# Performance work log

Hardware: AMD Instinct MI355X
Metric: run time of the kernel (lower is better)

## Reference

```python
import jax, jax.numpy as jnp
import numpy as np

B, H, NQ, NK, D = 256, 16, 49, 49, 64
SCALE = 1.0 / np.sqrt(D).astype(np.float32)
EPS = 1e-9  # matches kernel's 1/(l + 1e-9)


def setup_inputs() -> dict:
    key = jax.random.key(0)
    kq, kk, kv = jax.random.split(key, 3)
    q = jax.random.normal(kq, (B, H, NQ, D), dtype=jnp.float32)
    k = jax.random.normal(kk, (B, H, NK, D), dtype=jnp.float32)
    v = jax.random.normal(kv, (B, H, NK, D), dtype=jnp.float32)
    return {"q": q, "k": k, "v": v}


def reference(q, k, v):
    # scores: [B,H,Nq,Nk]
    s = jnp.einsum("bhqd,bhkd->bhqk", q, k) * SCALE
    m = jnp.max(s, axis=-1, keepdims=True)
    e = jnp.exp(s - m)
    l = jnp.sum(e, axis=-1, keepdims=True)
    p = e / (l + EPS)  # kernel divides by (l + 1e-9)
    out = jnp.einsum("bhqk,bhkd->bhqd", p, v)
    return out
```

## Files before the change

### kernel.cpp

```cpp
#include <hip/hip_runtime.h>


#define NQA 49
#define NKA 49
#define DD  64
#define ST  72

typedef __bf16 bf16x4 __attribute__((ext_vector_type(4)));
typedef __bf16 bf16x8 __attribute__((ext_vector_type(8)));
typedef float  f32x4  __attribute__((ext_vector_type(4)));

__global__ __launch_bounds__(256, 4)
void attn49_kernel(const float* __restrict__ Q, const float* __restrict__ K,
                   const float* __restrict__ V, float* __restrict__ O) {
    __shared__ __bf16 Qs[64 * ST];
    __shared__ __bf16 Ks[64 * ST];
    __shared__ __bf16 Vt[64 * ST];
    __shared__ __bf16 Ps[64 * ST];

    const int tid = threadIdx.x;
    const size_t base = (size_t)blockIdx.x * (NQA * DD);
    const float* Qg = Q + base;
    const float* Kg = K + base;
    const float* Vg = V + base;

    {
        const int f  = tid & 15;
        const int r0 = tid >> 4;
        #pragma unroll
        for (int it = 0; it < 4; ++it) {
            const int r = r0 + 16 * it;
            float4 qv = {0.f,0.f,0.f,0.f}, kv = {0.f,0.f,0.f,0.f};
            if (r < NQA) {
                qv = *(const float4*)(Qg + r * DD + 4 * f);
                kv = *(const float4*)(Kg + r * DD + 4 * f);
            }
            bf16x4 qb = { (__bf16)qv.x, (__bf16)qv.y, (__bf16)qv.z, (__bf16)qv.w };
            bf16x4 kb = { (__bf16)kv.x, (__bf16)kv.y, (__bf16)kv.z, (__bf16)kv.w };
            *(bf16x4*)&Qs[r * ST + 4 * f] = qb;
            *(bf16x4*)&Ks[r * ST + 4 * f] = kb;
        }
    }
    {
        const int k   = tid & 63;
        const int dg0 = tid >> 6;
        #pragma unroll
        for (int it = 0; it < 4; ++it) {
            const int dg = dg0 + 4 * it;
            float4 vv = {0.f,0.f,0.f,0.f};
            if (k < NKA) vv = *(const float4*)(Vg + k * DD + 4 * dg);
            Vt[(4*dg+0) * ST + k] = (__bf16)vv.x;
            Vt[(4*dg+1) * ST + k] = (__bf16)vv.y;
            Vt[(4*dg+2) * ST + k] = (__bf16)vv.z;
            Vt[(4*dg+3) * ST + k] = (__bf16)vv.w;
        }
    }
    __syncthreads();

    const int w  = tid >> 6;
    const int lr = tid & 15;
    const int lg = (tid >> 4) & 3;

    bf16x8 aq0 = *(const bf16x8*)&Qs[(16*w + lr) * ST      + 8*lg];
    bf16x8 aq1 = *(const bf16x8*)&Qs[(16*w + lr) * ST + 32 + 8*lg];
    f32x4 acc[4] = {};
    #pragma unroll
    for (int t = 0; t < 4; ++t) {
        bf16x8 b0 = *(const bf16x8*)&Ks[(16*t + lr) * ST      + 8*lg];
        bf16x8 b1 = *(const bf16x8*)&Ks[(16*t + lr) * ST + 32 + 8*lg];
        acc[t] = __builtin_amdgcn_mfma_f32_16x16x32_bf16(aq0, b0, acc[t], 0, 0, 0);
        acc[t] = __builtin_amdgcn_mfma_f32_16x16x32_bf16(aq1, b1, acc[t], 0, 0, 0);
    }

    float inv_l[4];
    #pragma unroll
    for (int i = 0; i < 4; ++i) {
        const int gq = 16*w + 4*lg + i;
        float s[4];
        float m = -1e30f;
        #pragma unroll
        for (int t = 0; t < 4; ++t) {
            float sv = acc[t][i] * 0.125f;
            if (16*t + lr > 48) sv = -1e30f;
            s[t] = sv;
            m = fmaxf(m, sv);
        }
        #pragma unroll
        for (int d = 1; d < 16; d <<= 1) m = fmaxf(m, __shfl_xor(m, d, 64));
        float e[4], sum = 0.f;
        #pragma unroll
        for (int t = 0; t < 4; ++t) {
            e[t] = (s[t] > -1e29f) ? __expf(s[t] - m) : 0.f;
            sum += e[t];
        }
        #pragma unroll
        for (int d = 1; d < 16; d <<= 1) sum += __shfl_xor(sum, d, 64);
        inv_l[i] = 1.f / (sum + 1e-9f);
        #pragma unroll
        for (int t = 0; t < 4; ++t)
            Ps[gq * ST + 16*t + lr] = (__bf16)e[t];
    }

    bf16x8 ap0 = *(const bf16x8*)&Ps[(16*w + lr) * ST      + 8*lg];
    bf16x8 ap1 = *(const bf16x8*)&Ps[(16*w + lr) * ST + 32 + 8*lg];
    f32x4 oacc[4] = {};
    #pragma unroll
    for (int t = 0; t < 4; ++t) {
        bf16x8 b0 = *(const bf16x8*)&Vt[(16*t + lr) * ST      + 8*lg];
        bf16x8 b1 = *(const bf16x8*)&Vt[(16*t + lr) * ST + 32 + 8*lg];
        oacc[t] = __builtin_amdgcn_mfma_f32_16x16x32_bf16(ap0, b0, oacc[t], 0, 0, 0);
        oacc[t] = __builtin_amdgcn_mfma_f32_16x16x32_bf16(ap1, b1, oacc[t], 0, 0, 0);
    }

    float* Og = O + base;
    #pragma unroll
    for (int i = 0; i < 4; ++i) {
        const int gq = 16*w + 4*lg + i;
        if (gq < NQA) {
            #pragma unroll
            for (int t = 0; t < 4; ++t)
                Og[gq * DD + 16*t + lr] = oacc[t][i] * inv_l[i];
        }
    }
}

extern "C" void kernel_launch(void* const* d_in, const int* in_sizes, int n_in,
                              void* d_out, int out_size, void* d_ws, size_t ws_size,
                              hipStream_t stream) {
    const float* q = (const float*)d_in[0];
    const float* k = (const float*)d_in[1];
    const float* v = (const float*)d_in[2];
    float* out = (float*)d_out;
    (void)in_sizes; (void)n_in; (void)out_size; (void)d_ws; (void)ws_size;
    attn49_kernel<<<dim3(4096), dim3(256), 0, stream>>>(q, k, v, out);
}
```

Measured before the change: 188.0 us.

## Load Q directly into MFMA registers and alias K/P shared buffers for occupancy

```diff
diff --git a/kernel.cpp b/kernel.cpp
--- a/kernel.cpp
+++ b/kernel.cpp
@@ -10,19 +10,34 @@
 typedef __bf16 bf16x8 __attribute__((ext_vector_type(8)));
 typedef float  f32x4  __attribute__((ext_vector_type(4)));
 
-__global__ __launch_bounds__(256, 4)
+__global__ __launch_bounds__(256, 8)
 void attn49_kernel(const float* __restrict__ Q, const float* __restrict__ K,
                    const float* __restrict__ V, float* __restrict__ O) {
-    __shared__ __bf16 Qs[64 * ST];
-    __shared__ __bf16 Ks[64 * ST];
+    __shared__ __bf16 KPs[64 * ST];
     __shared__ __bf16 Vt[64 * ST];
-    __shared__ __bf16 Ps[64 * ST];
 
     const int tid = threadIdx.x;
     const size_t base = (size_t)blockIdx.x * (NQA * DD);
-    const float* Qg = Q + base;
     const float* Kg = K + base;
     const float* Vg = V + base;
+
+    const int w  = tid >> 6;
+    const int lr = tid & 15;
+    const int lg = (tid >> 4) & 3;
+    const int qrow = 16 * w + lr;
+
+    bf16x8 aq0 = {}, aq1 = {};
+    if (qrow < NQA) {
+        const float* qp = Q + base + qrow * DD;
+        float4 q0 = *(const float4*)(qp +      8 * lg);
+        float4 q1 = *(const float4*)(qp +      8 * lg + 4);
+        float4 q2 = *(const float4*)(qp + 32 + 8 * lg);
+        float4 q3 = *(const float4*)(qp + 32 + 8 * lg + 4);
+        aq0 = (bf16x8){ (__bf16)q0.x,(__bf16)q0.y,(__bf16)q0.z,(__bf16)q0.w,
+                        (__bf16)q1.x,(__bf16)q1.y,(__bf16)q1.z,(__bf16)q1.w };
+        aq1 = (bf16x8){ (__bf16)q2.x,(__bf16)q2.y,(__bf16)q2.z,(__bf16)q2.w,
+                        (__bf16)q3.x,(__bf16)q3.y,(__bf16)q3.z,(__bf16)q3.w };
+    }
 
     {
         const int f  = tid & 15;
@@ -30,15 +45,10 @@
         #pragma unroll
         for (int it = 0; it < 4; ++it) {
             const int r = r0 + 16 * it;
-            float4 qv = {0.f,0.f,0.f,0.f}, kv = {0.f,0.f,0.f,0.f};
-            if (r < NQA) {
-                qv = *(const float4*)(Qg + r * DD + 4 * f);
-                kv = *(const float4*)(Kg + r * DD + 4 * f);
-            }
-            bf16x4 qb = { (__bf16)qv.x, (__bf16)qv.y, (__bf16)qv.z, (__bf16)qv.w };
+            float4 kv = {0.f,0.f,0.f,0.f};
+            if (r < NKA) kv = *(const float4*)(Kg + r * DD + 4 * f);
             bf16x4 kb = { (__bf16)kv.x, (__bf16)kv.y, (__bf16)kv.z, (__bf16)kv.w };
-            *(bf16x4*)&Qs[r * ST + 4 * f] = qb;
-            *(bf16x4*)&Ks[r * ST + 4 * f] = kb;
+            *(bf16x4*)&KPs[r * ST + 4 * f] = kb;
         }
     }
     {
@@ -57,20 +67,16 @@
     }
     __syncthreads();
 
-    const int w  = tid >> 6;
-    const int lr = tid & 15;
-    const int lg = (tid >> 4) & 3;
-
-    bf16x8 aq0 = *(const bf16x8*)&Qs[(16*w + lr) * ST      + 8*lg];
-    bf16x8 aq1 = *(const bf16x8*)&Qs[(16*w + lr) * ST + 32 + 8*lg];
     f32x4 acc[4] = {};
     #pragma unroll
     for (int t = 0; t < 4; ++t) {
-        bf16x8 b0 = *(const bf16x8*)&Ks[(16*t + lr) * ST      + 8*lg];
-        bf16x8 b1 = *(const bf16x8*)&Ks[(16*t + lr) * ST + 32 + 8*lg];
+        bf16x8 b0 = *(const bf16x8*)&KPs[(16*t + lr) * ST      + 8*lg];
+        bf16x8 b1 = *(const bf16x8*)&KPs[(16*t + lr) * ST + 32 + 8*lg];
         acc[t] = __builtin_amdgcn_mfma_f32_16x16x32_bf16(aq0, b0, acc[t], 0, 0, 0);
         acc[t] = __builtin_amdgcn_mfma_f32_16x16x32_bf16(aq1, b1, acc[t], 0, 0, 0);
     }
+
+    __syncthreads();
 
     float inv_l[4];
     #pragma unroll
@@ -98,11 +104,11 @@
         inv_l[i] = 1.f / (sum + 1e-9f);
         #pragma unroll
         for (int t = 0; t < 4; ++t)
-            Ps[gq * ST + 16*t + lr] = (__bf16)e[t];
+            KPs[gq * ST + 16*t + lr] = (__bf16)e[t];
     }
 
-    bf16x8 ap0 = *(const bf16x8*)&Ps[(16*w + lr) * ST      + 8*lg];
-    bf16x8 ap1 = *(const bf16x8*)&Ps[(16*w + lr) * ST + 32 + 8*lg];
+    bf16x8 ap0 = *(const bf16x8*)&KPs[(16*w + lr) * ST      + 8*lg];
+    bf16x8 ap1 = *(const bf16x8*)&KPs[(16*w + lr) * ST + 32 + 8*lg];
     f32x4 oacc[4] = {};
     #pragma unroll
     for (int t = 0; t < 4; ++t) {
```

Measured after the change: 187.4 us. About the same (-0.3%).
